# Optimization experiments

Hardware: AMD Instinct MI355X
Metric: run time of the kernel (lower is better)

Reference implementation:

```python
import jax, jax.numpy as jnp
import numpy as np

N_NODES = 100000
N_EDGES = 1600000
D = 64


def _sage_conv(x, src, dst, W_l, W_r, b):
    # PyG SAGEConv (aggr='mean'): out_i = W_l @ mean_{j in N(i)} x_j + W_r @ x_i + b
    n = x.shape[0]
    msgs = x[src]  # [E, D] gather of source-node features
    agg = jax.ops.segment_sum(msgs, dst, num_segments=n)  # [N, D]
    cnt = jax.ops.segment_sum(jnp.ones((src.shape[0],), x.dtype), dst, num_segments=n)
    mean = agg / jnp.maximum(cnt, 1.0)[:, None]
    return mean @ W_l.T + x @ W_r.T + b


def setup_inputs() -> dict:
    key = jax.random.key(0)
    ks = jax.random.split(key, 8)
    s = 1.0 / np.sqrt(D)
    x = jax.random.normal(ks[0], (N_NODES, D), dtype=jnp.float32)
    edge_index = jax.random.randint(ks[1], (2, N_EDGES), 0, N_NODES, dtype=jnp.int64)
    return {
        "x": x,
        "edge_index": edge_index,
        "W1_l": jax.random.normal(ks[2], (D, D), dtype=jnp.float32) * s,
        "W1_r": jax.random.normal(ks[3], (D, D), dtype=jnp.float32) * s,
        "b1": jnp.zeros((D,), dtype=jnp.float32),
        "W2_l": jax.random.normal(ks[4], (D, D), dtype=jnp.float32) * s,
        "W2_r": jax.random.normal(ks[5], (D, D), dtype=jnp.float32) * s,
        "b2": jnp.zeros((D,), dtype=jnp.float32),
    }


def reference(x, edge_index, W1_l, W1_r, b1, W2_l, W2_r, b2):
    src, dst = edge_index[0], edge_index[1]
    h = _sage_conv(x, src, dst, W1_l, W1_r, b1)
    h = jax.nn.relu(h)
    out = _sage_conv(h, src, dst, W2_l, W2_r, b2)
    return out
```

## Files before the change

kernel.cpp:

```cpp
#include <hip/hip_runtime.h>

#define D 64
#define BSHIFT 9
#define BNODES (1 << BSHIFT)
#define NBK_MAX 512

typedef __attribute__((ext_vector_type(8))) short bf16x8;
typedef __attribute__((ext_vector_type(4))) float f32x4;

__device__ __forceinline__ unsigned int f2bf_rne(float f) {
    unsigned int b = __float_as_uint(f);
    return (b + 0x7fffu + ((b >> 16) & 1u)) >> 16;
}
__device__ __forceinline__ unsigned int pack_bf(float lo, float hi) {
    return f2bf_rne(lo) | (f2bf_rne(hi) << 16);
}
__device__ __forceinline__ float bflo(unsigned int u) { return __uint_as_float(u << 16); }
__device__ __forceinline__ float bfhi(unsigned int u) { return __uint_as_float(u & 0xffff0000u); }

__global__ void zeroi_kernel(int* __restrict__ p, int n) {
    int i = blockIdx.x * blockDim.x + threadIdx.x;
    if (i < n) p[i] = 0;
}

__global__ void cast_kernel(const float4* __restrict__ xin, uint2* __restrict__ xb, int n4) {
    int i = blockIdx.x * blockDim.x + threadIdx.x;
    int stride = gridDim.x * blockDim.x;
    for (; i < n4; i += stride) {
        float4 v = xin[i];
        uint2 o;
        o.x = pack_bf(v.x, v.y);
        o.y = pack_bf(v.z, v.w);
        xb[i] = o;
    }
}

__global__ __launch_bounds__(256) void hist2_kernel(const int* __restrict__ dst,
                                                    int* __restrict__ cnt2,
                                                    int E, int NBK, int CE) {
    __shared__ int lh[NBK_MAX];
    for (int k = threadIdx.x; k < NBK; k += 256) lh[k] = 0;
    __syncthreads();
    int b = blockIdx.x, g = b & 7;
    int beg = b * CE, end = min(beg + CE, E);
    for (int e = beg + threadIdx.x; e < end; e += 256)
        atomicAdd(&lh[dst[e] >> BSHIFT], 1);
    __syncthreads();
    for (int k = threadIdx.x; k < NBK; k += 256)
        if (lh[k]) atomicAdd(&cnt2[(k << 3) | g], lh[k]);
}

__global__ __launch_bounds__(256) void scan2k_kernel(const int* __restrict__ cnt2,
                                                     int* __restrict__ cur2,
                                                     int* __restrict__ bstart, int NBK) {
    __shared__ int s[256];
    int n = NBK << 3;
    int tid = threadIdx.x;
    int base = tid * 8;
    int loc[8];
    int sum = 0;
    for (int j = 0; j < 8; ++j) {
        int idx = base + j;
        int v = (idx < n) ? cnt2[idx] : 0;
        loc[j] = sum;
        sum += v;
    }
    s[tid] = sum;
    __syncthreads();
    for (int off = 1; off < 256; off <<= 1) {
        int t = (tid >= off) ? s[tid - off] : 0;
        __syncthreads();
        s[tid] += t;
        __syncthreads();
    }
    int ebase = s[tid] - sum;
    for (int j = 0; j < 8; ++j) {
        int idx = base + j;
        if (idx < n) cur2[idx] = ebase + loc[j];
    }
    if (tid < NBK) bstart[tid] = ebase;
    if (tid == 0) bstart[NBK] = s[255];
}

__global__ __launch_bounds__(256) void binscatter_kernel(
    const int* __restrict__ src, const int* __restrict__ dst,
    int* __restrict__ cur2, unsigned int* __restrict__ pairs,
    int E, int NBK, int CE) {
    __shared__ int lh[NBK_MAX];
    __shared__ int lbase[NBK_MAX];
    for (int k = threadIdx.x; k < NBK; k += 256) lh[k] = 0;
    __syncthreads();
    int b = blockIdx.x, g = b & 7;
    int beg = b * CE, end = min(beg + CE, E);
    for (int e = beg + threadIdx.x; e < end; e += 256)
        atomicAdd(&lh[dst[e] >> BSHIFT], 1);
    __syncthreads();
    for (int k = threadIdx.x; k < NBK; k += 256) {
        int c = lh[k];
        if (c) lbase[k] = atomicAdd(&cur2[(k << 3) | g], c);
        lh[k] = 0;
    }
    __syncthreads();
    for (int e = beg + threadIdx.x; e < end; e += 256) {
        int d = dst[e];
        int k = d >> BSHIFT;
        int r = atomicAdd(&lh[k], 1);
        pairs[lbase[k] + r] = (unsigned int)src[e] | ((unsigned int)(d & (BNODES - 1)) << 17);
    }
}

__global__ __launch_bounds__(256) void csr_build_kernel(
    const unsigned int* __restrict__ pairs, const int* __restrict__ bstart,
    int* __restrict__ rowptr, int* __restrict__ csr, int N, int NBK) {
    __shared__ int lcnt[BNODES];
    __shared__ int lofs[BNODES];
    __shared__ int s[256];
    int k = blockIdx.x;
    int tid = threadIdx.x;
    int node0 = k << BSHIFT;
    int nnodes = min(BNODES, N - node0);
    int rbeg = bstart[k], rend = bstart[k + 1];

    for (int j = tid; j < BNODES; j += 256) lcnt[j] = 0;
    __syncthreads();
    for (int i = rbeg + tid; i < rend; i += 256)
        atomicAdd(&lcnt[pairs[i] >> 17], 1);
    __syncthreads();
    int v0 = lcnt[2 * tid], v1 = lcnt[2 * tid + 1];
    int ps = v0 + v1;
    s[tid] = ps;
    __syncthreads();
    for (int off = 1; off < 256; off <<= 1) {
        int t = (tid >= off) ? s[tid - off] : 0;
        __syncthreads();
        s[tid] += t;
        __syncthreads();
    }
    int ebase = s[tid] - ps;
    lofs[2 * tid] = ebase;
    lofs[2 * tid + 1] = ebase + v0;
    __syncthreads();
    for (int j = tid; j < nnodes; j += 256) {
        int p = rbeg + lofs[j];
        rowptr[node0 + j] = p;
        lcnt[j] = p;
    }
    if (k == NBK - 1 && tid == 0) rowptr[N] = rend;
    __syncthreads();
    for (int i = rbeg + tid; i < rend; i += 256) {
        unsigned int rec = pairs[i];
        int j = rec >> 17;
        int pos = atomicAdd(&lcnt[j], 1);
        csr[pos] = (int)(rec & 0x1FFFFu);
    }
}

__global__ __launch_bounds__(256) void agg_bf_kernel(
    const unsigned int* __restrict__ xb, const int* __restrict__ rowptr,
    const int* __restrict__ csr, unsigned int* __restrict__ meanb, int N) {
    int lane = threadIdx.x & 63;
    int q  = lane >> 4;
    int fl = lane & 15;
    int wid = blockIdx.x * (blockDim.x >> 6) + (threadIdx.x >> 6);
    int nwaves = gridDim.x * (blockDim.x >> 6);
    int nquads = (N + 3) >> 2;

    for (int p = wid; p < nquads; p += nwaves) {
        int node = p * 4 + q;
        bool valid = node < N;
        int beg = 0, end = 0;
        if (valid) { beg = rowptr[node]; end = rowptr[node + 1]; }
        float s0 = 0.f, s1 = 0.f, s2 = 0.f, s3 = 0.f;
        int j = beg;
        for (; j + 4 <= end; j += 4) {
            int i0 = csr[j], i1 = csr[j + 1], i2 = csr[j + 2], i3 = csr[j + 3];
            uint2 u0 = *(const uint2*)(xb + i0 * 32 + fl * 2);
            uint2 u1 = *(const uint2*)(xb + i1 * 32 + fl * 2);
            uint2 u2 = *(const uint2*)(xb + i2 * 32 + fl * 2);
            uint2 u3 = *(const uint2*)(xb + i3 * 32 + fl * 2);
            s0 += bflo(u0.x) + bflo(u1.x) + bflo(u2.x) + bflo(u3.x);
            s1 += bfhi(u0.x) + bfhi(u1.x) + bfhi(u2.x) + bfhi(u3.x);
            s2 += bflo(u0.y) + bflo(u1.y) + bflo(u2.y) + bflo(u3.y);
            s3 += bfhi(u0.y) + bfhi(u1.y) + bfhi(u2.y) + bfhi(u3.y);
        }
        for (; j < end; ++j) {
            uint2 u = *(const uint2*)(xb + csr[j] * 32 + fl * 2);
            s0 += bflo(u.x);
            s1 += bfhi(u.x);
            s2 += bflo(u.y);
            s3 += bfhi(u.y);
        }
        if (valid) {
            float inv = 1.0f / fmaxf((float)(end - beg), 1.0f);
            uint2 o;
            o.x = pack_bf(s0 * inv, s1 * inv);
            o.y = pack_bf(s2 * inv, s3 * inv);
            *(uint2*)(meanb + node * 32 + fl * 2) = o;
        }
    }
}

__global__ __launch_bounds__(256) void lin_mfma_kernel(
    const unsigned int* __restrict__ meanb, const unsigned int* __restrict__ xin,
    const float* __restrict__ Wl, const float* __restrict__ Wr,
    const float* __restrict__ bias,
    float* __restrict__ outf, unsigned int* __restrict__ outb, int N, int relu) {
    int tid = threadIdx.x;
    int ft   = tid >> 6;
    int lane = tid & 63;
    int lm   = lane & 15;
    int quad = lane >> 4;

    int f_a = ft * 16 + lm;
    bf16x8 wh[4], wlo[4];
#pragma unroll
    for (int s = 0; s < 4; ++s) {
        int k8 = s * 32 + quad * 8;
        const float* Wsrc = (k8 < 64) ? Wl : Wr;
        const float* p = Wsrc + f_a * 64 + (k8 & 63);
        float4 w0 = *(const float4*)p;
        float4 w1 = *(const float4*)(p + 4);
        float w[8] = {w0.x, w0.y, w0.z, w0.w, w1.x, w1.y, w1.z, w1.w};
        bf16x8 h, l;
#pragma unroll
        for (int j = 0; j < 8; ++j) {
            unsigned int hb = f2bf_rne(w[j]);
            float hf = __uint_as_float(hb << 16);
            unsigned int lb = f2bf_rne(w[j] - hf);
            h[j] = (short)hb;
            l[j] = (short)lb;
        }
        wh[s] = h;
        wlo[s] = l;
    }

    int node0 = blockIdx.x * 64;
    f32x4 acc[4];
#pragma unroll
    for (int nt = 0; nt < 4; ++nt) acc[nt] = (f32x4){0.f, 0.f, 0.f, 0.f};

#pragma unroll
    for (int nt = 0; nt < 4; ++nt) {
        int node = node0 + nt * 16 + lm;
        bool v = node < N;
        const unsigned int* mrow = meanb + (long long)node * 32;
        const unsigned int* xrow = xin   + (long long)node * 32;
#pragma unroll
        for (int s = 0; s < 4; ++s) {
            uint4 u = make_uint4(0u, 0u, 0u, 0u);
            if (v) {
                const unsigned int* srcrow = (s < 2) ? mrow : xrow;
                u = *(const uint4*)(srcrow + (s & 1) * 16 + quad * 4);
            }
            union { uint4 u4; bf16x8 v8; } cv;
            cv.u4 = u;
            acc[nt] = __builtin_amdgcn_mfma_f32_16x16x32_bf16(wh[s],  cv.v8, acc[nt], 0, 0, 0);
            acc[nt] = __builtin_amdgcn_mfma_f32_16x16x32_bf16(wlo[s], cv.v8, acc[nt], 0, 0, 0);
        }
    }

    int fb = ft * 16 + quad * 4;
    float4 bv = *(const float4*)(bias + fb);
#pragma unroll
    for (int nt = 0; nt < 4; ++nt) {
        int node = node0 + nt * 16 + lm;
        if (node >= N) continue;
        float r0 = acc[nt][0] + bv.x;
        float r1 = acc[nt][1] + bv.y;
        float r2 = acc[nt][2] + bv.z;
        float r3 = acc[nt][3] + bv.w;
        if (relu) {
            r0 = fmaxf(r0, 0.f); r1 = fmaxf(r1, 0.f);
            r2 = fmaxf(r2, 0.f); r3 = fmaxf(r3, 0.f);
        }
        if (outf) *(float4*)(outf + (long long)node * D + fb) = make_float4(r0, r1, r2, r3);
        if (outb) *(uint2*)(outb + (long long)node * 32 + (fb >> 1)) =
                      make_uint2(pack_bf(r0, r1), pack_bf(r2, r3));
    }
}

extern "C" void kernel_launch(void* const* d_in, const int* in_sizes, int n_in,
                              void* d_out, int out_size, void* d_ws, size_t ws_size,
                              hipStream_t stream) {
    const float* x   = (const float*)d_in[0];
    const int* ei    = (const int*)d_in[1];
    const float* W1l = (const float*)d_in[2];
    const float* W1r = (const float*)d_in[3];
    const float* b1  = (const float*)d_in[4];
    const float* W2l = (const float*)d_in[5];
    const float* W2r = (const float*)d_in[6];
    const float* b2  = (const float*)d_in[7];

    const int E = in_sizes[1] / 2;
    const int N = in_sizes[0] / D;
    const int* src  = ei;
    const int* dstp = ei + E;
    const int NBK = (N + BNODES - 1) >> BSHIFT;
    const int G1 = 512;
    const int CE = (E + G1 - 1) / G1;

    char* ws = (char*)d_ws;
    size_t off = 0;
    auto alloc = [&](size_t bytes) { void* p = ws + off; off = (off + bytes + 255) & ~(size_t)255; return p; };
    int* cnt2           = (int*)alloc((size_t)(NBK * 8) * 4);
    int* cur2           = (int*)alloc((size_t)(NBK * 8) * 4);
    int* bstart         = (int*)alloc((size_t)(NBK + 1) * 4);
    int* rowptr         = (int*)alloc((size_t)(N + 1) * 4);
    unsigned int* pairs = (unsigned int*)alloc((size_t)E * 4);
    int* csr            = (int*)alloc((size_t)E * 4);
    unsigned int* xb    = (unsigned int*)alloc((size_t)N * 32 * 4);
    unsigned int* meanb = (unsigned int*)alloc((size_t)N * 32 * 4);
    unsigned int* hb    = (unsigned int*)alloc((size_t)N * 32 * 4);

    float* out = (float*)d_out;

    cast_kernel<<<2048, 256, 0, stream>>>((const float4*)x, (uint2*)xb, N * 16);

    zeroi_kernel<<<(NBK * 8 + 255) / 256, 256, 0, stream>>>(cnt2, NBK * 8);
    hist2_kernel<<<G1, 256, 0, stream>>>(dstp, cnt2, E, NBK, CE);
    scan2k_kernel<<<1, 256, 0, stream>>>(cnt2, cur2, bstart, NBK);
    binscatter_kernel<<<G1, 256, 0, stream>>>(src, dstp, cur2, pairs, E, NBK, CE);
    csr_build_kernel<<<NBK, 256, 0, stream>>>(pairs, bstart, rowptr, csr, N, NBK);

    const int linGrid = (N + 63) / 64;

    agg_bf_kernel<<<4096, 256, 0, stream>>>(xb, rowptr, csr, meanb, N);
    lin_mfma_kernel<<<linGrid, 256, 0, stream>>>(meanb, xb, W1l, W1r, b1, nullptr, hb, N, 1);

    agg_bf_kernel<<<4096, 256, 0, stream>>>(hb, rowptr, csr, meanb, N);
    lin_mfma_kernel<<<linGrid, 256, 0, stream>>>(meanb, hb, W2l, W2r, b2, out, nullptr, N, 0);
}
```

Measured before the change: 271.3 us.

## Shrink CSR-build buckets, double binning grid, and unroll gather loop to 8

Reduces the destination bucket size from 512 to 128 nodes, so there are more, smaller buckets. The CSR build and scan kernels are reworked to handle this: a per-thread variable-width scan and a single-element-per-thread bucket scan. The binning grid is doubled to 1024 blocks, and the aggregation inner loop is unrolled to 8 neighbors to put more gathers in flight. The trade-offs are more global atomics on the bucket counters, a larger 32-entry scan array per thread, and higher register pressure in the aggregation loop.

```diff
diff --git a/kernel.cpp b/kernel.cpp
--- a/kernel.cpp
+++ b/kernel.cpp
@@ -1,9 +1,9 @@
 #include <hip/hip_runtime.h>
 
 #define D 64
-#define BSHIFT 9
+#define BSHIFT 7
 #define BNODES (1 << BSHIFT)
-#define NBK_MAX 512
+#define NBK_MAX 1024
 
 typedef __attribute__((ext_vector_type(8))) short bf16x8;
 typedef __attribute__((ext_vector_type(4))) float f32x4;
@@ -55,11 +55,12 @@
                                                      int* __restrict__ bstart, int NBK) {
     __shared__ int s[256];
     int n = NBK << 3;
+    int per = (n + 255) / 256;
     int tid = threadIdx.x;
-    int base = tid * 8;
-    int loc[8];
+    int base = tid * per;
+    int loc[32];
     int sum = 0;
-    for (int j = 0; j < 8; ++j) {
+    for (int j = 0; j < per; ++j) {
         int idx = base + j;
         int v = (idx < n) ? cnt2[idx] : 0;
         loc[j] = sum;
@@ -74,11 +75,14 @@
         __syncthreads();
     }
     int ebase = s[tid] - sum;
-    for (int j = 0; j < 8; ++j) {
+    for (int j = 0; j < per; ++j) {
         int idx = base + j;
-        if (idx < n) cur2[idx] = ebase + loc[j];
-    }
-    if (tid < NBK) bstart[tid] = ebase;
+        if (idx < n) {
+            int e = ebase + loc[j];
+            cur2[idx] = e;
+            if ((idx & 7) == 0) bstart[idx >> 3] = e;
+        }
+    }
     if (tid == 0) bstart[NBK] = s[255];
 }
 
@@ -114,36 +118,33 @@
     int* __restrict__ rowptr, int* __restrict__ csr, int N, int NBK) {
     __shared__ int lcnt[BNODES];
     __shared__ int lofs[BNODES];
-    __shared__ int s[256];
+    __shared__ int s2[BNODES];
     int k = blockIdx.x;
     int tid = threadIdx.x;
     int node0 = k << BSHIFT;
     int nnodes = min(BNODES, N - node0);
     int rbeg = bstart[k], rend = bstart[k + 1];
 
-    for (int j = tid; j < BNODES; j += 256) lcnt[j] = 0;
+    if (tid < BNODES) lcnt[tid] = 0;
     __syncthreads();
     for (int i = rbeg + tid; i < rend; i += 256)
         atomicAdd(&lcnt[pairs[i] >> 17], 1);
     __syncthreads();
-    int v0 = lcnt[2 * tid], v1 = lcnt[2 * tid + 1];
-    int ps = v0 + v1;
-    s[tid] = ps;
-    __syncthreads();
-    for (int off = 1; off < 256; off <<= 1) {
-        int t = (tid >= off) ? s[tid - off] : 0;
+    if (tid < BNODES) s2[tid] = lcnt[tid];
+    __syncthreads();
+    for (int off = 1; off < BNODES; off <<= 1) {
+        int t = 0;
+        if (tid < BNODES && tid >= off) t = s2[tid - off];
         __syncthreads();
-        s[tid] += t;
+        if (tid < BNODES && tid >= off) s2[tid] += t;
         __syncthreads();
     }
-    int ebase = s[tid] - ps;
-    lofs[2 * tid] = ebase;
-    lofs[2 * tid + 1] = ebase + v0;
-    __syncthreads();
-    for (int j = tid; j < nnodes; j += 256) {
-        int p = rbeg + lofs[j];
-        rowptr[node0 + j] = p;
-        lcnt[j] = p;
+    if (tid < BNODES) lofs[tid] = s2[tid] - lcnt[tid];
+    __syncthreads();
+    if (tid < nnodes) {
+        int p = rbeg + lofs[tid];
+        rowptr[node0 + tid] = p;
+        lcnt[tid] = p;
     }
     if (k == NBK - 1 && tid == 0) rowptr[N] = rend;
     __syncthreads();
@@ -172,6 +173,26 @@
         if (valid) { beg = rowptr[node]; end = rowptr[node + 1]; }
         float s0 = 0.f, s1 = 0.f, s2 = 0.f, s3 = 0.f;
         int j = beg;
+        for (; j + 8 <= end; j += 8) {
+            int i0 = csr[j],     i1 = csr[j + 1], i2 = csr[j + 2], i3 = csr[j + 3];
+            int i4 = csr[j + 4], i5 = csr[j + 5], i6 = csr[j + 6], i7 = csr[j + 7];
+            uint2 u0 = *(const uint2*)(xb + i0 * 32 + fl * 2);
+            uint2 u1 = *(const uint2*)(xb + i1 * 32 + fl * 2);
+            uint2 u2 = *(const uint2*)(xb + i2 * 32 + fl * 2);
+            uint2 u3 = *(const uint2*)(xb + i3 * 32 + fl * 2);
+            uint2 u4 = *(const uint2*)(xb + i4 * 32 + fl * 2);
+            uint2 u5 = *(const uint2*)(xb + i5 * 32 + fl * 2);
+            uint2 u6 = *(const uint2*)(xb + i6 * 32 + fl * 2);
+            uint2 u7 = *(const uint2*)(xb + i7 * 32 + fl * 2);
+            s0 += bflo(u0.x) + bflo(u1.x) + bflo(u2.x) + bflo(u3.x)
+                + bflo(u4.x) + bflo(u5.x) + bflo(u6.x) + bflo(u7.x);
+            s1 += bfhi(u0.x) + bfhi(u1.x) + bfhi(u2.x) + bfhi(u3.x)
+                + bfhi(u4.x) + bfhi(u5.x) + bfhi(u6.x) + bfhi(u7.x);
+            s2 += bflo(u0.y) + bflo(u1.y) + bflo(u2.y) + bflo(u3.y)
+                + bflo(u4.y) + bflo(u5.y) + bflo(u6.y) + bflo(u7.y);
+            s3 += bfhi(u0.y) + bfhi(u1.y) + bfhi(u2.y) + bfhi(u3.y)
+                + bfhi(u4.y) + bfhi(u5.y) + bfhi(u6.y) + bfhi(u7.y);
+        }
         for (; j + 4 <= end; j += 4) {
             int i0 = csr[j], i1 = csr[j + 1], i2 = csr[j + 2], i3 = csr[j + 3];
             uint2 u0 = *(const uint2*)(xb + i0 * 32 + fl * 2);
@@ -296,7 +317,7 @@
     const int* src  = ei;
     const int* dstp = ei + E;
     const int NBK = (N + BNODES - 1) >> BSHIFT;
-    const int G1 = 512;
+    const int G1 = 1024;
     const int CE = (E + G1 - 1) / G1;
 
     char* ws = (char*)d_ws;
```

After: 325.2 us. 19.9% more time.
